# Optimization experiments

Hardware: AMD Instinct MI355X
Metric: run time of the kernel (lower is better)

## Reference

```python
import jax, jax.numpy as jnp
import numpy as np

# Config (matches init_kwargs)
B, S = 2, 2048            # 2 packed sequences of 2048 tokens (prefill)
HQ, HK, D = 32, 8, 128    # GQA: 32 query heads, 8 kv heads
G = HQ // HK              # group size 4
WINDOW = 1024             # sliding window
THETA = 10000.0


def setup_inputs() -> dict:
    key = jax.random.key(0)
    kq, kk, kv = jax.random.split(key, 3)
    n_tokens = B * S
    query = jax.random.normal(kq, (n_tokens, HQ * D), dtype=jnp.float32)
    key_t = jax.random.normal(kk, (n_tokens, HK * D), dtype=jnp.float32)
    value = jax.random.normal(kv, (n_tokens, HK * D), dtype=jnp.float32)
    # per-sequence positions restart at 0 for each packed sequence
    positions = jnp.tile(jnp.arange(S, dtype=jnp.int32), B)
    return {"query": query, "key": key_t, "value": value, "positions": positions}


def _rope(x, positions):
    # x: [B, S, H, D]; rotate-half (NeoX) RoPE
    half = D // 2
    inv_freq = 1.0 / (THETA ** (jnp.arange(0, half, dtype=jnp.float32) / half))
    ang = positions.astype(jnp.float32)[:, None] * inv_freq[None, :]   # [B*S, D/2]
    cos = jnp.cos(ang).reshape(B, S, 1, half)
    sin = jnp.sin(ang).reshape(B, S, 1, half)
    x1, x2 = x[..., :half], x[..., half:]
    return jnp.concatenate([x1 * cos - x2 * sin, x2 * cos + x1 * sin], axis=-1)


def reference(query, key, value, positions):
    q = query.reshape(B, S, HQ, D)
    k = key.reshape(B, S, HK, D)
    v = value.reshape(B, S, HK, D)
    q = _rope(q, positions)
    k = _rope(k, positions)
    # GQA: split q heads into [HK, G]
    qg = q.reshape(B, S, HK, G, D)
    scale = 1.0 / jnp.sqrt(jnp.float32(D))
    # scores: [B, HK, G, Sq, Skv]
    scores = jnp.einsum('bqhgd,bshd->bhgqs', qg, k) * scale
    i = jnp.arange(S)[:, None]
    j = jnp.arange(S)[None, :]
    # causal + sliding window: j <= i and i - j < WINDOW
    mask = (j <= i) & ((i - j) < WINDOW)
    scores = jnp.where(mask[None, None, None], scores, jnp.float32(-1e30))
    attn = jax.nn.softmax(scores, axis=-1)
    out = jnp.einsum('bhgqs,bshd->bqhgd', attn, v)   # [B, Sq, HK, G, D]
    return out.reshape(B * S, HQ * D)
```

## Files before the change

kernel.cpp:

```cpp
#include <hip/hip_runtime.h>
#include <stdint.h>

#define NB 2
#define NS 2048
#define NHK 8
#define ND 128
#define NWIN 1024

using bf16x8 = __bf16 __attribute__((ext_vector_type(8)));
using f32x4  = float  __attribute__((ext_vector_type(4)));
using f32x2  = float  __attribute__((ext_vector_type(2)));
using f32x8  = float  __attribute__((ext_vector_type(8)));
using u16x8  = unsigned short __attribute__((ext_vector_type(8)));
using u32x4  = unsigned int   __attribute__((ext_vector_type(4)));

#define L2_10K (13.287712379549449f / 64.0f)
#define MASKV (-3.0e38f)

static __device__ __forceinline__ float ex2(float x) {
  return __builtin_amdgcn_exp2f(x);
}

static __device__ __forceinline__ unsigned short f2bf(float x) {
  unsigned int u = __builtin_bit_cast(unsigned int, x);
  u += 0x7FFFu + ((u >> 16) & 1u);
  return (unsigned short)(u >> 16);
}

static __device__ __forceinline__ unsigned int cvtpk(float lo, float hi) {
  unsigned int r;
  asm("v_cvt_pk_bf16_f32 %0, %1, %2" : "=v"(r) : "v"(lo), "v"(hi));
  return r;
}

static __device__ __forceinline__ void gll16(const void* g, void* l) {
  __builtin_amdgcn_global_load_lds(
      (const __attribute__((address_space(1))) void*)g,
      (__attribute__((address_space(3))) void*)l, 16, 0, 0);
}

#define MFMA16(a, b, c) __builtin_amdgcn_mfma_f32_16x16x32_bf16((a), (b), (c), 0, 0, 0)

__global__ __launch_bounds__(64) void build_tab(float* __restrict__ tab) {
  const int p = blockIdx.x, f = threadIdx.x;
  float s, c;
  __sincosf((float)p * ex2(-(float)f * L2_10K), &s, &c);
  tab[(size_t)p * 128 + f] = c;
  tab[(size_t)p * 128 + 64 + f] = s;
}

__global__ __launch_bounds__(256) void prepass(
    const float* __restrict__ kin, const float* __restrict__ vin,
    const int* __restrict__ pos, const float* __restrict__ tab,
    unsigned short* __restrict__ kimg, unsigned short* __restrict__ vimg) {
  const int bid = blockIdx.x;
  const int ti = bid & 63, gidx = bid >> 6;
  const int hk = gidx & 7, b = gidx >> 3;
  const int t = threadIdx.x;

  unsigned short* kout = kimg + (size_t)bid * 4096;
#pragma unroll
  for (int uu = 0; uu < 2; ++uu) {
    const int u = t * 2 + uu;
    const int j = u >> 4;
    const int d0 = ((u & 15) << 3) ^ ((j & 7) << 3);
    const int tok = (b << 11) + (ti << 5) + j;
    const float* kp = kin + (size_t)tok * (NHK * ND) + hk * ND;
    f32x8 a = *(const f32x8*)(kp + d0);
    f32x8 p = *(const f32x8*)(kp + (d0 ^ 64));
    const float* tr = tab + (size_t)(pos[tok] & 2047) * 128 + (d0 & 63);
    f32x8 c8 = *(const f32x8*)tr;
    f32x8 s8 = *(const f32x8*)(tr + 64);
    u16x8 o;
#pragma unroll
    for (int i = 0; i < 8; ++i) {
      float val = (d0 < 64) ? (a[i] * c8[i] - p[i] * s8[i])
                            : (a[i] * c8[i] + p[i] * s8[i]);
      o[i] = f2bf(val);
    }
    *(u16x8*)(kout + (size_t)u * 8) = o;
  }

  unsigned short* vout = vimg + (size_t)bid * 4096;
  {
    const int d0 = (t >> 2) << 1;
    const int kp4 = t & 3;
    const int tok0 = (b << 11) + (ti << 5) + (kp4 << 3);
    const float* vp = vin + (size_t)tok0 * (NHK * ND) + hk * ND + d0;
    u16x8 lo, hi;
#pragma unroll
    for (int i = 0; i < 8; ++i) {
      f32x2 r = *(const f32x2*)(vp + (size_t)i * (NHK * ND));
      lo[i] = f2bf(r[0]);
      hi[i] = f2bf(r[1]);
    }
    const int sub = kp4 ^ ((d0 >> 1) & 3);
    *(u16x8*)(vout + d0 * 32 + sub * 8) = lo;
    *(u16x8*)(vout + (d0 + 1) * 32 + sub * 8) = hi;
  }
}

template <bool PRE>
__global__ __launch_bounds__(256, 3) void attn_fwd(
    const float* __restrict__ qin, const float* __restrict__ kin,
    const float* __restrict__ vin, const int* __restrict__ pos,
    const char* __restrict__ kimg, const char* __restrict__ vimg,
    const float* __restrict__ tab, float* __restrict__ out) {
  __shared__ __align__(16) char Kb[3][8192];
  __shared__ __align__(16) char Vb[3][8192];

  const int B = blockIdx.x;
  const int group = (B & 7) + ((B >> 9) << 3);
  const int qt = 63 - ((B >> 3) & 63);
  const int hk = group & 7, b = group >> 3;

  const int tid = threadIdx.x;
  const int w = tid >> 6, lane = tid & 63, h = lane >> 4, ln = lane & 15;
  const int g = w;
  const int q0b = qt << 5;
  int lo = q0b - (NWIN - 1);
  if (lo < 0) lo = 0;
  lo &= ~31;
  const int ti0 = lo >> 5;
  const int nt = (q0b >> 5) - ti0 + 1;

  const size_t gbase = (size_t)group * 64 * 8192;
  const char* kg = PRE ? kimg + gbase + (size_t)(w * 128 + lane) * 16 : nullptr;
  const char* vg = PRE ? vimg + gbase + (size_t)(w * 128 + lane) * 16 : nullptr;

  auto stage = [&](int sl, int ti) {
    if constexpr (PRE) {
      const char* ksrc = kg + (size_t)ti * 8192;
      const char* vsrc = vg + (size_t)ti * 8192;
      char* kd = &Kb[sl][w * 2048];
      char* vd = &Vb[sl][w * 2048];
      gll16(ksrc, kd);
      gll16(ksrc + 1024, kd + 1024);
      gll16(vsrc, vd);
      gll16(vsrc + 1024, vd + 1024);
    } else {
      const int j = tid >> 3;
      const int du = (tid & 7) << 4;
      const int tok = (b << 11) + (ti << 5) + j;
      const float* kp = kin + (size_t)tok * (NHK * ND) + hk * ND;
      const float pj = (float)pos[tok];
#pragma unroll
      for (int gq = 0; gq < 2; ++gq) {
        const int dd = du + gq * 8;
        f32x8 a = *(const f32x8*)(kp + dd);
        f32x8 p = *(const f32x8*)(kp + (dd ^ 64));
        u16x8 o;
#pragma unroll
        for (int i = 0; i < 8; ++i) {
          float s, c;
          __sincosf(pj * ex2(-(float)((dd & 63) + i) * L2_10K), &s, &c);
          float val = (dd < 64) ? (a[i] * c - p[i] * s) : (a[i] * c + p[i] * s);
          o[i] = f2bf(val);
        }
        *(u16x8*)(&Kb[sl][((j << 8) + (dd << 1)) ^ ((j & 7) << 4)]) = o;
      }
      const int d0 = (tid >> 2) << 1;
      const int kp4 = tid & 3;
      const float* vp = vin + (size_t)((b << 11) + (ti << 5) + (kp4 << 3)) * (NHK * ND) + hk * ND + d0;
      u16x8 lov, hiv;
#pragma unroll
      for (int i = 0; i < 8; ++i) {
        f32x2 r = *(const f32x2*)(vp + (size_t)i * (NHK * ND));
        lov[i] = f2bf(r[0]);
        hiv[i] = f2bf(r[1]);
      }
      const int sub = kp4 ^ ((d0 >> 1) & 3);
      unsigned short* vb16 = (unsigned short*)Vb[sl];
      *(u16x8*)(vb16 + d0 * 32 + sub * 8) = lov;
      *(u16x8*)(vb16 + (d0 + 1) * 32 + sub * 8) = hiv;
    }
  };

  stage(0, ti0);
  if (nt > 1) stage(1, ti0 + 1);

  const float QSC = 0.08838834764831845f * 1.4426950408889634f;
  bf16x8 qfr[2][4];
#pragma unroll
  for (int hf = 0; hf < 2; ++hf) {
    const int qrow = q0b + hf * 16 + ln;
    const size_t tokq = (size_t)(b << 11) + qrow;
    const float* qp = qin + tokq * 4096 + (hk * 4 + g) * 128;
    const int posq = pos[tokq] & 2047;
#pragma unroll
    for (int pp = 0; pp < 2; ++pp) {
      const int rr = (pp << 5) + (h << 3);
      f32x8 lo8 = *(const f32x8*)(qp + rr);
      f32x8 hi8 = *(const f32x8*)(qp + rr + 64);
      f32x8 cc, ss;
      if constexpr (PRE) {
        const float* tp = tab + (size_t)posq * 128 + rr;
        cc = *(const f32x8*)tp;
        ss = *(const f32x8*)(tp + 64);
      } else {
        const float pf = (float)posq;
#pragma unroll
        for (int i = 0; i < 8; ++i) {
          float s, c;
          __sincosf(pf * ex2(-(float)(rr + i) * L2_10K), &s, &c);
          cc[i] = c;
          ss[i] = s;
        }
      }
      u16x8 ulo, uhi;
#pragma unroll
      for (int i = 0; i < 8; ++i) {
        ulo[i] = f2bf((lo8[i] * cc[i] - hi8[i] * ss[i]) * QSC);
        uhi[i] = f2bf((hi8[i] * cc[i] + lo8[i] * ss[i]) * QSC);
      }
      qfr[hf][pp] = __builtin_bit_cast(bf16x8, ulo);
      qfr[hf][2 + pp] = __builtin_bit_cast(bf16x8, uhi);
    }
  }

  asm volatile("s_waitcnt vmcnt(0)" ::: "memory");

  f32x4 Oc[2][8] = {};
  float msh[2] = {-1e30f, -1e30f};
  float lsum[2] = {};
  const int sw = (ln & 7) << 4;
  const int vsub = (h ^ ((ln >> 1) & 3)) << 4;
  int s0 = 0, s1 = 1, s2 = 2;

  for (int t = 0; t < nt; ++t) {
    if constexpr (PRE) {
      if (t + 1 < nt) asm volatile("s_waitcnt vmcnt(4)" ::: "memory");
      else            asm volatile("s_waitcnt vmcnt(0)" ::: "memory");
    } else {
      asm volatile("s_waitcnt vmcnt(0) lgkmcnt(0)" ::: "memory");
    }
    __builtin_amdgcn_s_barrier();
    __builtin_amdgcn_sched_barrier(0);
    if (t + 2 < nt) stage(s2, ti0 + t + 2);

    const int j0 = (ti0 + t) << 5;
    const char* KB = Kb[s0];

    f32x4 sT[2][2] = {};
    __builtin_amdgcn_s_setprio(1);
#pragma unroll
    for (int c = 0; c < 4; ++c) {
      const bf16x8 k0 = *(const bf16x8*)(
          KB + (((ln << 8) + (c << 6) + (h << 4)) ^ sw));
      const bf16x8 k1 = *(const bf16x8*)(
          KB + ((((16 + ln) << 8) + (c << 6) + (h << 4)) ^ sw));
      sT[0][0] = MFMA16(k0, qfr[0][c], sT[0][0]);
      sT[0][1] = MFMA16(k1, qfr[0][c], sT[0][1]);
      sT[1][0] = MFMA16(k0, qfr[1][c], sT[1][0]);
      sT[1][1] = MFMA16(k1, qfr[1][c], sT[1][1]);
    }
    __builtin_amdgcn_s_setprio(0);

    if ((j0 >= q0b) || (j0 < q0b - 992)) {
#pragma unroll
      for (int qh = 0; qh < 2; ++qh) {
        const int irow = q0b + qh * 16 + ln;
#pragma unroll
        for (int ki = 0; ki < 2; ++ki)
#pragma unroll
          for (int r = 0; r < 4; ++r) {
            const int j = j0 + ki * 16 + (h << 2) + r;
            if (!(j <= irow && irow - j < NWIN)) sT[qh][ki][r] = MASKV;
          }
      }
    }

    float pm[2];
#pragma unroll
    for (int qh = 0; qh < 2; ++qh) {
      const f32x4 a0 = sT[qh][0], a1 = sT[qh][1];
      pm[qh] = fmaxf(fmaxf(fmaxf(a0[0], a0[1]), fmaxf(a0[2], a0[3])),
                     fmaxf(fmaxf(a1[0], a1[1]), fmaxf(a1[2], a1[3])));
    }
    const float ov = fmaxf(pm[0] - msh[0], pm[1] - msh[1]);
    if (__any(ov > 8.0f)) {
#pragma unroll
      for (int qh = 0; qh < 2; ++qh) {
        float M = pm[qh];
        M = fmaxf(M, __shfl_xor(M, 16));
        M = fmaxf(M, __shfl_xor(M, 32));
        const float mn = fmaxf(msh[qh], M);
        const float co = ex2(msh[qh] - mn);
        msh[qh] = mn;
        lsum[qh] *= co;
        float coO[4];
#pragma unroll
        for (int r = 0; r < 4; ++r) coO[r] = __shfl(co, (h << 2) + r);
#pragma unroll
        for (int db = 0; db < 8; ++db)
#pragma unroll
          for (int r = 0; r < 4; ++r) Oc[qh][db][r] *= coO[r];
      }
    }

    bf16x8 pa[2];
#pragma unroll
    for (int qh = 0; qh < 2; ++qh) {
#pragma unroll
      for (int ki = 0; ki < 2; ++ki)
#pragma unroll
        for (int r = 0; r < 4; ++r)
          sT[qh][ki][r] = ex2(sT[qh][ki][r] - msh[qh]);
      lsum[qh] += ((sT[qh][0][0] + sT[qh][0][1]) + (sT[qh][0][2] + sT[qh][0][3])) +
                  ((sT[qh][1][0] + sT[qh][1][1]) + (sT[qh][1][2] + sT[qh][1][3]));
      unsigned int A = cvtpk(sT[qh][0][0], sT[qh][0][1]);
      unsigned int Bk = cvtpk(sT[qh][0][2], sT[qh][0][3]);
      unsigned int C = cvtpk(sT[qh][1][0], sT[qh][1][1]);
      unsigned int D = cvtpk(sT[qh][1][2], sT[qh][1][3]);
      asm volatile("v_permlane32_swap_b32 %0, %1" : "+v"(A), "+v"(C));
      asm volatile("v_permlane16_swap_b32 %0, %1" : "+v"(A), "+v"(C));
      asm volatile("v_permlane32_swap_b32 %0, %1" : "+v"(Bk), "+v"(D));
      asm volatile("v_permlane16_swap_b32 %0, %1" : "+v"(Bk), "+v"(D));
      u32x4 pk4 = {A, Bk, C, D};
      pa[qh] = __builtin_bit_cast(bf16x8, pk4);
    }

    const char* VB = Vb[s0];
    __builtin_amdgcn_s_setprio(1);
#pragma unroll
    for (int db = 0; db < 8; ++db) {
      const bf16x8 vv = *(const bf16x8*)(VB + (db << 10) + (ln << 6) + vsub);
      Oc[0][db] = MFMA16(pa[0], vv, Oc[0][db]);
      Oc[1][db] = MFMA16(pa[1], vv, Oc[1][db]);
    }
    __builtin_amdgcn_s_setprio(0);

    const int tmp = s0;
    s0 = s1; s1 = s2; s2 = tmp;
  }

#pragma unroll
  for (int qh = 0; qh < 2; ++qh) {
    float ls = lsum[qh];
    ls += __shfl_xor(ls, 16);
    ls += __shfl_xor(ls, 32);
#pragma unroll
    for (int r = 0; r < 4; ++r) {
      const float rl = 1.0f / __shfl(ls, (h << 2) + r);
      const int irow = q0b + qh * 16 + (h << 2) + r;
      float* op = out + ((size_t)(b << 11) + irow) * 4096 + (hk * 4 + g) * 128 + ln;
#pragma unroll
      for (int db = 0; db < 8; ++db) op[db * 16] = Oc[qh][db][r] * rl;
    }
  }
}

extern "C" void kernel_launch(void* const* d_in, const int* in_sizes, int n_in,
                              void* d_out, int out_size, void* d_ws, size_t ws_size,
                              hipStream_t stream) {
  const float* q = (const float*)d_in[0];
  const float* k = (const float*)d_in[1];
  const float* v = (const float*)d_in[2];
  const int* pos = (const int*)d_in[3];
  float* out = (float*)d_out;

  const size_t TAB = (size_t)2048 * 128 * 4;
  const size_t KIMG = (size_t)16 * 64 * 8192;
  const size_t need = TAB + 2 * KIMG;

  if (ws_size >= need) {
    float* tab = (float*)d_ws;
    char* kimg = (char*)d_ws + TAB;
    char* vimg = kimg + KIMG;
    build_tab<<<2048, 64, 0, stream>>>(tab);
    prepass<<<1024, 256, 0, stream>>>(k, v, pos, tab,
                                      (unsigned short*)kimg, (unsigned short*)vimg);
    attn_fwd<true><<<1024, 256, 0, stream>>>(q, k, v, pos, kimg, vimg, tab, out);
  } else {
    attn_fwd<false><<<1024, 256, 0, stream>>>(q, k, v, pos, nullptr, nullptr, nullptr, out);
  }
}
```

Measured before the change: 95.92 us.

## Switch attention inner loop to 32x32x16 MFMA with double-buffered LDS

Replaces the 16x16x32 bf16 MFMA tiling with 32x32x16 MFMA for both QK^T and PV. Each lane now owns one query row, so the softmax max and sum reductions need only one cross-half shuffle, and output is written with vectorized float4 stores. The LDS pipeline goes from triple to double buffering with a __syncthreads per tile. That frees LDS for an occupancy hint of 4 blocks per CU but loses one stage of prefetch depth. Query tiles are also interleaved long and short to balance work across blocks.

```diff
diff --git a/kernel.cpp b/kernel.cpp
--- a/kernel.cpp
+++ b/kernel.cpp
@@ -11,6 +11,7 @@
 using f32x4  = float  __attribute__((ext_vector_type(4)));
 using f32x2  = float  __attribute__((ext_vector_type(2)));
 using f32x8  = float  __attribute__((ext_vector_type(8)));
+using f32x16 = float  __attribute__((ext_vector_type(16)));
 using u16x8  = unsigned short __attribute__((ext_vector_type(8)));
 using u32x4  = unsigned int   __attribute__((ext_vector_type(4)));
 
@@ -39,7 +40,7 @@
       (__attribute__((address_space(3))) void*)l, 16, 0, 0);
 }
 
-#define MFMA16(a, b, c) __builtin_amdgcn_mfma_f32_16x16x32_bf16((a), (b), (c), 0, 0, 0)
+#define MFMA32(a, b, c) __builtin_amdgcn_mfma_f32_32x32x16_bf16((a), (b), (c), 0, 0, 0)
 
 __global__ __launch_bounds__(64) void build_tab(float* __restrict__ tab) {
   const int p = blockIdx.x, f = threadIdx.x;
@@ -101,21 +102,23 @@
 }
 
 template <bool PRE>
-__global__ __launch_bounds__(256, 3) void attn_fwd(
+__global__ __launch_bounds__(256, 4) void attn_fwd(
     const float* __restrict__ qin, const float* __restrict__ kin,
     const float* __restrict__ vin, const int* __restrict__ pos,
     const char* __restrict__ kimg, const char* __restrict__ vimg,
     const float* __restrict__ tab, float* __restrict__ out) {
-  __shared__ __align__(16) char Kb[3][8192];
-  __shared__ __align__(16) char Vb[3][8192];
+  __shared__ __align__(16) char Kb[2][8192];
+  __shared__ __align__(16) char Vb[2][8192];
 
   const int B = blockIdx.x;
   const int group = (B & 7) + ((B >> 9) << 3);
-  const int qt = 63 - ((B >> 3) & 63);
+  const int qi = (B >> 3) & 63;
+  const int qt = (qi & 1) ? (qi >> 1) : (63 - (qi >> 1));
   const int hk = group & 7, b = group >> 3;
 
   const int tid = threadIdx.x;
-  const int w = tid >> 6, lane = tid & 63, h = lane >> 4, ln = lane & 15;
+  const int w = tid >> 6, lane = tid & 63;
+  const int r32 = lane & 31, hi = lane >> 5;
   const int g = w;
   const int q0b = qt << 5;
   int lo = q0b - (NWIN - 1);
@@ -124,20 +127,17 @@
   const int ti0 = lo >> 5;
   const int nt = (q0b >> 5) - ti0 + 1;
 
-  const size_t gbase = (size_t)group * 64 * 8192;
-  const char* kg = PRE ? kimg + gbase + (size_t)(w * 128 + lane) * 16 : nullptr;
-  const char* vg = PRE ? vimg + gbase + (size_t)(w * 128 + lane) * 16 : nullptr;
+  const int gvoff = group * 64 * 8192 + (w * 128 + lane) * 16;
 
   auto stage = [&](int sl, int ti) {
     if constexpr (PRE) {
-      const char* ksrc = kg + (size_t)ti * 8192;
-      const char* vsrc = vg + (size_t)ti * 8192;
+      const int off = gvoff + ti * 8192;
       char* kd = &Kb[sl][w * 2048];
       char* vd = &Vb[sl][w * 2048];
-      gll16(ksrc, kd);
-      gll16(ksrc + 1024, kd + 1024);
-      gll16(vsrc, vd);
-      gll16(vsrc + 1024, vd + 1024);
+      gll16(kimg + off, kd);
+      gll16(kimg + off + 1024, kd + 1024);
+      gll16(vimg + off, vd);
+      gll16(vimg + off + 1024, vd + 1024);
     } else {
       const int j = tid >> 3;
       const int du = (tid & 7) << 4;
@@ -177,24 +177,22 @@
   };
 
   stage(0, ti0);
-  if (nt > 1) stage(1, ti0 + 1);
 
   const float QSC = 0.08838834764831845f * 1.4426950408889634f;
-  bf16x8 qfr[2][4];
-#pragma unroll
-  for (int hf = 0; hf < 2; ++hf) {
-    const int qrow = q0b + hf * 16 + ln;
+  bf16x8 qfr[8];
+  {
+    const int qrow = q0b + r32;
     const size_t tokq = (size_t)(b << 11) + qrow;
     const float* qp = qin + tokq * 4096 + (hk * 4 + g) * 128;
     const int posq = pos[tokq] & 2047;
 #pragma unroll
-    for (int pp = 0; pp < 2; ++pp) {
-      const int rr = (pp << 5) + (h << 3);
-      f32x8 lo8 = *(const f32x8*)(qp + rr);
-      f32x8 hi8 = *(const f32x8*)(qp + rr + 64);
+    for (int m = 0; m < 4; ++m) {
+      const int dlo = (m << 4) + (hi << 3);
+      f32x8 lo8 = *(const f32x8*)(qp + dlo);
+      f32x8 hi8 = *(const f32x8*)(qp + dlo + 64);
       f32x8 cc, ss;
       if constexpr (PRE) {
-        const float* tp = tab + (size_t)posq * 128 + rr;
+        const float* tp = tab + (size_t)posq * 128 + dlo;
         cc = *(const f32x8*)tp;
         ss = *(const f32x8*)(tp + 64);
       } else {
@@ -202,7 +200,7 @@
 #pragma unroll
         for (int i = 0; i < 8; ++i) {
           float s, c;
-          __sincosf(pf * ex2(-(float)(rr + i) * L2_10K), &s, &c);
+          __sincosf(pf * ex2(-(float)(dlo + i) * L2_10K), &s, &c);
           cc[i] = c;
           ss[i] = s;
         }
@@ -213,141 +211,99 @@
         ulo[i] = f2bf((lo8[i] * cc[i] - hi8[i] * ss[i]) * QSC);
         uhi[i] = f2bf((hi8[i] * cc[i] + lo8[i] * ss[i]) * QSC);
       }
-      qfr[hf][pp] = __builtin_bit_cast(bf16x8, ulo);
-      qfr[hf][2 + pp] = __builtin_bit_cast(bf16x8, uhi);
-    }
-  }
-
-  asm volatile("s_waitcnt vmcnt(0)" ::: "memory");
-
-  f32x4 Oc[2][8] = {};
-  float msh[2] = {-1e30f, -1e30f};
-  float lsum[2] = {};
-  const int sw = (ln & 7) << 4;
-  const int vsub = (h ^ ((ln >> 1) & 3)) << 4;
-  int s0 = 0, s1 = 1, s2 = 2;
+      qfr[m] = __builtin_bit_cast(bf16x8, ulo);
+      qfr[m + 4] = __builtin_bit_cast(bf16x8, uhi);
+    }
+  }
+
+  f32x16 Oc[4] = {};
+  float msh = -1e30f;
+  float lsum = 0.0f;
+
+  const int kx = (r32 << 8) | ((hi ^ (r32 & 1)) << 4) | (((r32 & 7) >> 1) << 5);
+  const int vsz = (r32 >> 1) & 3;
+  const int vbase0 = r32 * 64;
 
   for (int t = 0; t < nt; ++t) {
-    if constexpr (PRE) {
-      if (t + 1 < nt) asm volatile("s_waitcnt vmcnt(4)" ::: "memory");
-      else            asm volatile("s_waitcnt vmcnt(0)" ::: "memory");
-    } else {
-      asm volatile("s_waitcnt vmcnt(0) lgkmcnt(0)" ::: "memory");
-    }
-    __builtin_amdgcn_s_barrier();
-    __builtin_amdgcn_sched_barrier(0);
-    if (t + 2 < nt) stage(s2, ti0 + t + 2);
+    __syncthreads();
+    if (t + 1 < nt) stage((t + 1) & 1, ti0 + t + 1);
 
     const int j0 = (ti0 + t) << 5;
-    const char* KB = Kb[s0];
-
-    f32x4 sT[2][2] = {};
+    const char* KB = Kb[t & 1];
+    const char* VB = Vb[t & 1];
+
+    f32x16 sT = {};
     __builtin_amdgcn_s_setprio(1);
 #pragma unroll
-    for (int c = 0; c < 4; ++c) {
-      const bf16x8 k0 = *(const bf16x8*)(
-          KB + (((ln << 8) + (c << 6) + (h << 4)) ^ sw));
-      const bf16x8 k1 = *(const bf16x8*)(
-          KB + ((((16 + ln) << 8) + (c << 6) + (h << 4)) ^ sw));
-      sT[0][0] = MFMA16(k0, qfr[0][c], sT[0][0]);
-      sT[0][1] = MFMA16(k1, qfr[0][c], sT[0][1]);
-      sT[1][0] = MFMA16(k0, qfr[1][c], sT[1][0]);
-      sT[1][1] = MFMA16(k1, qfr[1][c], sT[1][1]);
+    for (int m = 0; m < 8; ++m) {
+      const bf16x8 kf = *(const bf16x8*)(KB + (kx ^ (m << 5)));
+      sT = MFMA32(kf, qfr[m], sT);
     }
     __builtin_amdgcn_s_setprio(0);
 
     if ((j0 >= q0b) || (j0 < q0b - 992)) {
-#pragma unroll
-      for (int qh = 0; qh < 2; ++qh) {
-        const int irow = q0b + qh * 16 + ln;
-#pragma unroll
-        for (int ki = 0; ki < 2; ++ki)
-#pragma unroll
-          for (int r = 0; r < 4; ++r) {
-            const int j = j0 + ki * 16 + (h << 2) + r;
-            if (!(j <= irow && irow - j < NWIN)) sT[qh][ki][r] = MASKV;
-          }
-      }
-    }
-
-    float pm[2];
-#pragma unroll
-    for (int qh = 0; qh < 2; ++qh) {
-      const f32x4 a0 = sT[qh][0], a1 = sT[qh][1];
-      pm[qh] = fmaxf(fmaxf(fmaxf(a0[0], a0[1]), fmaxf(a0[2], a0[3])),
-                     fmaxf(fmaxf(a1[0], a1[1]), fmaxf(a1[2], a1[3])));
-    }
-    const float ov = fmaxf(pm[0] - msh[0], pm[1] - msh[1]);
-    if (__any(ov > 8.0f)) {
-#pragma unroll
-      for (int qh = 0; qh < 2; ++qh) {
-        float M = pm[qh];
-        M = fmaxf(M, __shfl_xor(M, 16));
-        M = fmaxf(M, __shfl_xor(M, 32));
-        const float mn = fmaxf(msh[qh], M);
-        const float co = ex2(msh[qh] - mn);
-        msh[qh] = mn;
-        lsum[qh] *= co;
-        float coO[4];
-#pragma unroll
-        for (int r = 0; r < 4; ++r) coO[r] = __shfl(co, (h << 2) + r);
-#pragma unroll
-        for (int db = 0; db < 8; ++db)
-#pragma unroll
-          for (int r = 0; r < 4; ++r) Oc[qh][db][r] *= coO[r];
-      }
-    }
-
-    bf16x8 pa[2];
-#pragma unroll
-    for (int qh = 0; qh < 2; ++qh) {
-#pragma unroll
-      for (int ki = 0; ki < 2; ++ki)
-#pragma unroll
-        for (int r = 0; r < 4; ++r)
-          sT[qh][ki][r] = ex2(sT[qh][ki][r] - msh[qh]);
-      lsum[qh] += ((sT[qh][0][0] + sT[qh][0][1]) + (sT[qh][0][2] + sT[qh][0][3])) +
-                  ((sT[qh][1][0] + sT[qh][1][1]) + (sT[qh][1][2] + sT[qh][1][3]));
-      unsigned int A = cvtpk(sT[qh][0][0], sT[qh][0][1]);
-      unsigned int Bk = cvtpk(sT[qh][0][2], sT[qh][0][3]);
-      unsigned int C = cvtpk(sT[qh][1][0], sT[qh][1][1]);
-      unsigned int D = cvtpk(sT[qh][1][2], sT[qh][1][3]);
-      asm volatile("v_permlane32_swap_b32 %0, %1" : "+v"(A), "+v"(C));
-      asm volatile("v_permlane16_swap_b32 %0, %1" : "+v"(A), "+v"(C));
-      asm volatile("v_permlane32_swap_b32 %0, %1" : "+v"(Bk), "+v"(D));
-      asm volatile("v_permlane16_swap_b32 %0, %1" : "+v"(Bk), "+v"(D));
-      u32x4 pk4 = {A, Bk, C, D};
-      pa[qh] = __builtin_bit_cast(bf16x8, pk4);
-    }
-
-    const char* VB = Vb[s0];
+      const int irow = q0b + r32;
+#pragma unroll
+      for (int r = 0; r < 16; ++r) {
+        const int j = j0 + (r & 3) + 8 * (r >> 2) + 4 * hi;
+        if (!(j <= irow && irow - j < NWIN)) sT[r] = MASKV;
+      }
+    }
+
+    float pm = sT[0];
+#pragma unroll
+    for (int r = 1; r < 16; ++r) pm = fmaxf(pm, sT[r]);
+    if (__any(pm - msh > 8.0f)) {
+      float M = fmaxf(pm, __shfl_xor(pm, 32));
+      const float mn = fmaxf(msh, M);
+      const float co = ex2(msh - mn);
+      msh = mn;
+      lsum *= co;
+#pragma unroll
+      for (int dt = 0; dt < 4; ++dt)
+#pragma unroll
+        for (int r = 0; r < 16; ++r) Oc[dt][r] *= co;
+    }
+#pragma unroll
+    for (int r = 0; r < 16; ++r) sT[r] = ex2(sT[r] - msh);
+    lsum += (((sT[0] + sT[1]) + (sT[2] + sT[3])) + ((sT[4] + sT[5]) + (sT[6] + sT[7]))) +
+            (((sT[8] + sT[9]) + (sT[10] + sT[11])) + ((sT[12] + sT[13]) + (sT[14] + sT[15])));
+
+    unsigned int A00 = cvtpk(sT[0], sT[1]),   A01 = cvtpk(sT[2], sT[3]);
+    unsigned int A10 = cvtpk(sT[4], sT[5]),   A11 = cvtpk(sT[6], sT[7]);
+    unsigned int A20 = cvtpk(sT[8], sT[9]),   A21 = cvtpk(sT[10], sT[11]);
+    unsigned int A30 = cvtpk(sT[12], sT[13]), A31 = cvtpk(sT[14], sT[15]);
+
     __builtin_amdgcn_s_setprio(1);
 #pragma unroll
-    for (int db = 0; db < 8; ++db) {
-      const bf16x8 vv = *(const bf16x8*)(VB + (db << 10) + (ln << 6) + vsub);
-      Oc[0][db] = MFMA16(pa[0], vv, Oc[0][db]);
-      Oc[1][db] = MFMA16(pa[1], vv, Oc[1][db]);
+    for (int ks = 0; ks < 2; ++ks) {
+      unsigned int w0 = ks ? A20 : A00, w1 = ks ? A21 : A01;
+      unsigned int w2 = ks ? A30 : A10, w3 = ks ? A31 : A11;
+      asm volatile("v_permlane32_swap_b32 %0, %1" : "+v"(w0), "+v"(w2));
+      asm volatile("v_permlane32_swap_b32 %0, %1" : "+v"(w1), "+v"(w3));
+      u32x4 pk4 = {w0, w1, w2, w3};
+      const bf16x8 pb = __builtin_bit_cast(bf16x8, pk4);
+      const int vslot = (((ks << 1) | hi) ^ vsz) << 4;
+#pragma unroll
+      for (int dt = 0; dt < 4; ++dt) {
+        const bf16x8 vf = *(const bf16x8*)(VB + (dt << 11) + vbase0 + vslot);
+        Oc[dt] = MFMA32(vf, pb, Oc[dt]);
+      }
     }
     __builtin_amdgcn_s_setprio(0);
-
-    const int tmp = s0;
-    s0 = s1; s1 = s2; s2 = tmp;
-  }
-
-#pragma unroll
-  for (int qh = 0; qh < 2; ++qh) {
-    float ls = lsum[qh];
-    ls += __shfl_xor(ls, 16);
-    ls += __shfl_xor(ls, 32);
-#pragma unroll
-    for (int r = 0; r < 4; ++r) {
-      const float rl = 1.0f / __shfl(ls, (h << 2) + r);
-      const int irow = q0b + qh * 16 + (h << 2) + r;
-      float* op = out + ((size_t)(b << 11) + irow) * 4096 + (hk * 4 + g) * 128 + ln;
-#pragma unroll
-      for (int db = 0; db < 8; ++db) op[db * 16] = Oc[qh][db][r] * rl;
-    }
-  }
+  }
+
+  float ls = lsum + __shfl_xor(lsum, 32);
+  const float rl = 1.0f / ls;
+  float* op = out + ((size_t)(b << 11) + q0b + r32) * 4096 + (hk * 4 + g) * 128 + (hi << 2);
+#pragma unroll
+  for (int dt = 0; dt < 4; ++dt)
+#pragma unroll
+    for (int s = 0; s < 4; ++s) {
+      f32x4 o = {Oc[dt][4 * s + 0] * rl, Oc[dt][4 * s + 1] * rl,
+                 Oc[dt][4 * s + 2] * rl, Oc[dt][4 * s + 3] * rl};
+      *(f32x4*)(op + (dt << 5) + (s << 3)) = o;
+    }
 }
 
 extern "C" void kernel_launch(void* const* d_in, const int* in_sizes, int n_in,
```

Result: slower. 137.7 us (+43.5%).

## Load V fragments directly from global into registers, double-buffer K only

Applied to the files above, without the earlier changes.

V tiles are no longer staged through LDS. Each lane now loads its bf16 V fragments straight from the preformatted global image into registers, split into two halves around the softmax. K staging drops from a triple-buffer ring to a double buffer with a full vmcnt(0) wait and syncthreads each iteration. The aim is to cut LDS footprint and LDS traffic, but the V global-load latency is now exposed inside the loop and the prefetch depth is reduced.

```diff
diff --git a/kernel.cpp b/kernel.cpp
--- a/kernel.cpp
+++ b/kernel.cpp
@@ -106,8 +106,7 @@
     const float* __restrict__ vin, const int* __restrict__ pos,
     const char* __restrict__ kimg, const char* __restrict__ vimg,
     const float* __restrict__ tab, float* __restrict__ out) {
-  __shared__ __align__(16) char Kb[3][8192];
-  __shared__ __align__(16) char Vb[3][8192];
+  __shared__ __align__(16) char Kb[2][8192];
 
   const int B = blockIdx.x;
   const int group = (B & 7) + ((B >> 9) << 3);
@@ -126,18 +125,14 @@
 
   const size_t gbase = (size_t)group * 64 * 8192;
   const char* kg = PRE ? kimg + gbase + (size_t)(w * 128 + lane) * 16 : nullptr;
-  const char* vg = PRE ? vimg + gbase + (size_t)(w * 128 + lane) * 16 : nullptr;
+  const char* vgb = PRE ? vimg + gbase : nullptr;
 
   auto stage = [&](int sl, int ti) {
     if constexpr (PRE) {
       const char* ksrc = kg + (size_t)ti * 8192;
-      const char* vsrc = vg + (size_t)ti * 8192;
       char* kd = &Kb[sl][w * 2048];
-      char* vd = &Vb[sl][w * 2048];
       gll16(ksrc, kd);
       gll16(ksrc + 1024, kd + 1024);
-      gll16(vsrc, vd);
-      gll16(vsrc + 1024, vd + 1024);
     } else {
       const int j = tid >> 3;
       const int du = (tid & 7) << 4;
@@ -159,25 +154,10 @@
         }
         *(u16x8*)(&Kb[sl][((j << 8) + (dd << 1)) ^ ((j & 7) << 4)]) = o;
       }
-      const int d0 = (tid >> 2) << 1;
-      const int kp4 = tid & 3;
-      const float* vp = vin + (size_t)((b << 11) + (ti << 5) + (kp4 << 3)) * (NHK * ND) + hk * ND + d0;
-      u16x8 lov, hiv;
-#pragma unroll
-      for (int i = 0; i < 8; ++i) {
-        f32x2 r = *(const f32x2*)(vp + (size_t)i * (NHK * ND));
-        lov[i] = f2bf(r[0]);
-        hiv[i] = f2bf(r[1]);
-      }
-      const int sub = kp4 ^ ((d0 >> 1) & 3);
-      unsigned short* vb16 = (unsigned short*)Vb[sl];
-      *(u16x8*)(vb16 + d0 * 32 + sub * 8) = lov;
-      *(u16x8*)(vb16 + (d0 + 1) * 32 + sub * 8) = hiv;
     }
   };
 
   stage(0, ti0);
-  if (nt > 1) stage(1, ti0 + 1);
 
   const float QSC = 0.08838834764831845f * 1.4426950408889634f;
   bf16x8 qfr[2][4];
@@ -218,28 +198,37 @@
     }
   }
 
-  asm volatile("s_waitcnt vmcnt(0)" ::: "memory");
-
   f32x4 Oc[2][8] = {};
   float msh[2] = {-1e30f, -1e30f};
   float lsum[2] = {};
   const int sw = (ln & 7) << 4;
-  const int vsub = (h ^ ((ln >> 1) & 3)) << 4;
-  int s0 = 0, s1 = 1, s2 = 2;
+  const int voff = (ln << 6) + ((h ^ ((ln >> 1) & 3)) << 4);
 
   for (int t = 0; t < nt; ++t) {
+    asm volatile("s_waitcnt vmcnt(0)" ::: "memory");
+    __syncthreads();
+    if (t + 1 < nt) stage((t + 1) & 1, ti0 + t + 1);
+
+    const int j0 = (ti0 + t) << 5;
+    const char* KB = Kb[t & 1];
+    const char* vt = PRE ? vgb + (size_t)(ti0 + t) * 8192 : nullptr;
+
+    bf16x8 vf[8];
     if constexpr (PRE) {
-      if (t + 1 < nt) asm volatile("s_waitcnt vmcnt(4)" ::: "memory");
-      else            asm volatile("s_waitcnt vmcnt(0)" ::: "memory");
+#pragma unroll
+      for (int db = 0; db < 4; ++db)
+        vf[db] = *(const bf16x8*)(vt + (db << 10) + voff);
     } else {
-      asm volatile("s_waitcnt vmcnt(0) lgkmcnt(0)" ::: "memory");
-    }
-    __builtin_amdgcn_s_barrier();
-    __builtin_amdgcn_sched_barrier(0);
-    if (t + 2 < nt) stage(s2, ti0 + t + 2);
-
-    const int j0 = (ti0 + t) << 5;
-    const char* KB = Kb[s0];
+#pragma unroll
+      for (int db = 0; db < 4; ++db) {
+        u16x8 o;
+#pragma unroll
+        for (int i = 0; i < 8; ++i)
+          o[i] = f2bf(vin[(size_t)((b << 11) + j0 + (h << 3) + i) * (NHK * ND) +
+                          hk * ND + (db << 4) + ln]);
+        vf[db] = __builtin_bit_cast(bf16x8, o);
+      }
+    }
 
     f32x4 sT[2][2] = {};
     __builtin_amdgcn_s_setprio(1);
@@ -320,18 +309,29 @@
       pa[qh] = __builtin_bit_cast(bf16x8, pk4);
     }
 
-    const char* VB = Vb[s0];
+    if constexpr (PRE) {
+#pragma unroll
+      for (int db = 4; db < 8; ++db)
+        vf[db] = *(const bf16x8*)(vt + (db << 10) + voff);
+    } else {
+#pragma unroll
+      for (int db = 4; db < 8; ++db) {
+        u16x8 o;
+#pragma unroll
+        for (int i = 0; i < 8; ++i)
+          o[i] = f2bf(vin[(size_t)((b << 11) + j0 + (h << 3) + i) * (NHK * ND) +
+                          hk * ND + (db << 4) + ln]);
+        vf[db] = __builtin_bit_cast(bf16x8, o);
+      }
+    }
+
     __builtin_amdgcn_s_setprio(1);
 #pragma unroll
     for (int db = 0; db < 8; ++db) {
-      const bf16x8 vv = *(const bf16x8*)(VB + (db << 10) + (ln << 6) + vsub);
-      Oc[0][db] = MFMA16(pa[0], vv, Oc[0][db]);
-      Oc[1][db] = MFMA16(pa[1], vv, Oc[1][db]);
+      Oc[0][db] = MFMA16(pa[0], vf[db], Oc[0][db]);
+      Oc[1][db] = MFMA16(pa[1], vf[db], Oc[1][db]);
     }
     __builtin_amdgcn_s_setprio(0);
-
-    const int tmp = s0;
-    s0 = s1; s1 = s2; s2 = tmp;
   }
 
 #pragma unroll
```

After: 103.3 us. 7.7% more time.

## Pair short and long causal query tiles per block and double-buffer K/V

Applied to the files above, without the earlier changes.

The grid shrinks from 1024 to 768 blocks. Each of the first 16 units per group handles two query tiles, a short early one (qt=u) and a long late one (qt=31-u), so the ramp-up region of the causal mask is balanced. The remaining units handle one full-window tile each. The K/V shared staging drops from triple to double buffering, which frees LDS but waits on all outstanding loads plus a full __syncthreads every iteration, reducing load/compute overlap. The intent is to even out per-block work across the causal/windowed workload.

```diff
diff --git a/kernel.cpp b/kernel.cpp
--- a/kernel.cpp
+++ b/kernel.cpp
@@ -106,23 +106,22 @@
     const float* __restrict__ vin, const int* __restrict__ pos,
     const char* __restrict__ kimg, const char* __restrict__ vimg,
     const float* __restrict__ tab, float* __restrict__ out) {
-  __shared__ __align__(16) char Kb[3][8192];
-  __shared__ __align__(16) char Vb[3][8192];
+  __shared__ __align__(16) char Kb[2][8192];
+  __shared__ __align__(16) char Vb[2][8192];
 
   const int B = blockIdx.x;
-  const int group = (B & 7) + ((B >> 9) << 3);
-  const int qt = 63 - ((B >> 3) & 63);
+  const int xcd = B & 7;
+  const int i96 = B >> 3;
+  const int group = xcd + ((i96 >= 48) ? 8 : 0);
+  const int unit = (i96 >= 48) ? i96 - 48 : i96;
   const int hk = group & 7, b = group >> 3;
+  const int isPair = unit < 16;
+  const int qtA = isPair ? unit : unit + 16;
+  const int qtB = 31 - unit;
 
   const int tid = threadIdx.x;
   const int w = tid >> 6, lane = tid & 63, h = lane >> 4, ln = lane & 15;
   const int g = w;
-  const int q0b = qt << 5;
-  int lo = q0b - (NWIN - 1);
-  if (lo < 0) lo = 0;
-  lo &= ~31;
-  const int ti0 = lo >> 5;
-  const int nt = (q0b >> 5) - ti0 + 1;
 
   const size_t gbase = (size_t)group * 64 * 8192;
   const char* kg = PRE ? kimg + gbase + (size_t)(w * 128 + lane) * 16 : nullptr;
@@ -176,176 +175,178 @@
     }
   };
 
-  stage(0, ti0);
-  if (nt > 1) stage(1, ti0 + 1);
-
   const float QSC = 0.08838834764831845f * 1.4426950408889634f;
-  bf16x8 qfr[2][4];
-#pragma unroll
-  for (int hf = 0; hf < 2; ++hf) {
-    const int qrow = q0b + hf * 16 + ln;
-    const size_t tokq = (size_t)(b << 11) + qrow;
-    const float* qp = qin + tokq * 4096 + (hk * 4 + g) * 128;
-    const int posq = pos[tokq] & 2047;
-#pragma unroll
-    for (int pp = 0; pp < 2; ++pp) {
-      const int rr = (pp << 5) + (h << 3);
-      f32x8 lo8 = *(const f32x8*)(qp + rr);
-      f32x8 hi8 = *(const f32x8*)(qp + rr + 64);
-      f32x8 cc, ss;
-      if constexpr (PRE) {
-        const float* tp = tab + (size_t)posq * 128 + rr;
-        cc = *(const f32x8*)tp;
-        ss = *(const f32x8*)(tp + 64);
-      } else {
-        const float pf = (float)posq;
-#pragma unroll
-        for (int i = 0; i < 8; ++i) {
-          float s, c;
-          __sincosf(pf * ex2(-(float)(rr + i) * L2_10K), &s, &c);
-          cc[i] = c;
-          ss[i] = s;
-        }
-      }
-      u16x8 ulo, uhi;
-#pragma unroll
-      for (int i = 0; i < 8; ++i) {
-        ulo[i] = f2bf((lo8[i] * cc[i] - hi8[i] * ss[i]) * QSC);
-        uhi[i] = f2bf((hi8[i] * cc[i] + lo8[i] * ss[i]) * QSC);
-      }
-      qfr[hf][pp] = __builtin_bit_cast(bf16x8, ulo);
-      qfr[hf][2 + pp] = __builtin_bit_cast(bf16x8, uhi);
-    }
-  }
-
-  asm volatile("s_waitcnt vmcnt(0)" ::: "memory");
-
-  f32x4 Oc[2][8] = {};
-  float msh[2] = {-1e30f, -1e30f};
-  float lsum[2] = {};
   const int sw = (ln & 7) << 4;
   const int vsub = (h ^ ((ln >> 1) & 3)) << 4;
-  int s0 = 0, s1 = 1, s2 = 2;
-
-  for (int t = 0; t < nt; ++t) {
-    if constexpr (PRE) {
-      if (t + 1 < nt) asm volatile("s_waitcnt vmcnt(4)" ::: "memory");
-      else            asm volatile("s_waitcnt vmcnt(0)" ::: "memory");
-    } else {
-      asm volatile("s_waitcnt vmcnt(0) lgkmcnt(0)" ::: "memory");
-    }
-    __builtin_amdgcn_s_barrier();
-    __builtin_amdgcn_sched_barrier(0);
-    if (t + 2 < nt) stage(s2, ti0 + t + 2);
-
-    const int j0 = (ti0 + t) << 5;
-    const char* KB = Kb[s0];
-
-    f32x4 sT[2][2] = {};
-    __builtin_amdgcn_s_setprio(1);
-#pragma unroll
-    for (int c = 0; c < 4; ++c) {
-      const bf16x8 k0 = *(const bf16x8*)(
-          KB + (((ln << 8) + (c << 6) + (h << 4)) ^ sw));
-      const bf16x8 k1 = *(const bf16x8*)(
-          KB + ((((16 + ln) << 8) + (c << 6) + (h << 4)) ^ sw));
-      sT[0][0] = MFMA16(k0, qfr[0][c], sT[0][0]);
-      sT[0][1] = MFMA16(k1, qfr[0][c], sT[0][1]);
-      sT[1][0] = MFMA16(k0, qfr[1][c], sT[1][0]);
-      sT[1][1] = MFMA16(k1, qfr[1][c], sT[1][1]);
-    }
-    __builtin_amdgcn_s_setprio(0);
-
-    if ((j0 >= q0b) || (j0 < q0b - 992)) {
+
+#pragma unroll 1
+  for (int seg = 0; seg < 2; ++seg) {
+    if (seg == 1 && !isPair) break;
+    const int qt = seg ? qtB : qtA;
+    const int q0b = qt << 5;
+    int lo = q0b - (NWIN - 1);
+    if (lo < 0) lo = 0;
+    lo &= ~31;
+    const int ti0 = lo >> 5;
+    const int nt = (q0b >> 5) - ti0 + 1;
+
+    __syncthreads();
+    stage(0, ti0);
+
+    bf16x8 qfr[2][4];
+#pragma unroll
+    for (int hf = 0; hf < 2; ++hf) {
+      const int qrow = q0b + hf * 16 + ln;
+      const size_t tokq = (size_t)(b << 11) + qrow;
+      const float* qp = qin + tokq * 4096 + (hk * 4 + g) * 128;
+      const int posq = pos[tokq] & 2047;
+#pragma unroll
+      for (int pp = 0; pp < 2; ++pp) {
+        const int rr = (pp << 5) + (h << 3);
+        f32x8 lo8 = *(const f32x8*)(qp + rr);
+        f32x8 hi8 = *(const f32x8*)(qp + rr + 64);
+        f32x8 cc, ss;
+        if constexpr (PRE) {
+          const float* tp = tab + (size_t)posq * 128 + rr;
+          cc = *(const f32x8*)tp;
+          ss = *(const f32x8*)(tp + 64);
+        } else {
+          const float pf = (float)posq;
+#pragma unroll
+          for (int i = 0; i < 8; ++i) {
+            float s, c;
+            __sincosf(pf * ex2(-(float)(rr + i) * L2_10K), &s, &c);
+            cc[i] = c;
+            ss[i] = s;
+          }
+        }
+        u16x8 ulo, uhi;
+#pragma unroll
+        for (int i = 0; i < 8; ++i) {
+          ulo[i] = f2bf((lo8[i] * cc[i] - hi8[i] * ss[i]) * QSC);
+          uhi[i] = f2bf((hi8[i] * cc[i] + lo8[i] * ss[i]) * QSC);
+        }
+        qfr[hf][pp] = __builtin_bit_cast(bf16x8, ulo);
+        qfr[hf][2 + pp] = __builtin_bit_cast(bf16x8, uhi);
+      }
+    }
+
+    f32x4 Oc[2][8] = {};
+    float msh[2] = {-1e30f, -1e30f};
+    float lsum[2] = {};
+
+#pragma unroll 1
+    for (int t = 0; t < nt; ++t) {
+      asm volatile("s_waitcnt vmcnt(0)" ::: "memory");
+      __syncthreads();
+      if (t + 1 < nt) stage((t + 1) & 1, ti0 + t + 1);
+
+      const int j0 = (ti0 + t) << 5;
+      const char* KB = Kb[t & 1];
+
+      f32x4 sT[2][2] = {};
+      __builtin_amdgcn_s_setprio(1);
+#pragma unroll
+      for (int c = 0; c < 4; ++c) {
+        const bf16x8 k0 = *(const bf16x8*)(
+            KB + (((ln << 8) + (c << 6) + (h << 4)) ^ sw));
+        const bf16x8 k1 = *(const bf16x8*)(
+            KB + ((((16 + ln) << 8) + (c << 6) + (h << 4)) ^ sw));
+        sT[0][0] = MFMA16(k0, qfr[0][c], sT[0][0]);
+        sT[0][1] = MFMA16(k1, qfr[0][c], sT[0][1]);
+        sT[1][0] = MFMA16(k0, qfr[1][c], sT[1][0]);
+        sT[1][1] = MFMA16(k1, qfr[1][c], sT[1][1]);
+      }
+      __builtin_amdgcn_s_setprio(0);
+
+      if ((j0 >= q0b) || (j0 < q0b - 992)) {
+#pragma unroll
+        for (int qh = 0; qh < 2; ++qh) {
+          const int irow = q0b + qh * 16 + ln;
+#pragma unroll
+          for (int ki = 0; ki < 2; ++ki)
+#pragma unroll
+            for (int r = 0; r < 4; ++r) {
+              const int j = j0 + ki * 16 + (h << 2) + r;
+              if (!(j <= irow && irow - j < NWIN)) sT[qh][ki][r] = MASKV;
+            }
+        }
+      }
+
+      float pm[2];
 #pragma unroll
       for (int qh = 0; qh < 2; ++qh) {
-        const int irow = q0b + qh * 16 + ln;
+        const f32x4 a0 = sT[qh][0], a1 = sT[qh][1];
+        pm[qh] = fmaxf(fmaxf(fmaxf(a0[0], a0[1]), fmaxf(a0[2], a0[3])),
+                       fmaxf(fmaxf(a1[0], a1[1]), fmaxf(a1[2], a1[3])));
+      }
+      const float ov = fmaxf(pm[0] - msh[0], pm[1] - msh[1]);
+      if (__any(ov > 8.0f)) {
+#pragma unroll
+        for (int qh = 0; qh < 2; ++qh) {
+          float M = pm[qh];
+          M = fmaxf(M, __shfl_xor(M, 16));
+          M = fmaxf(M, __shfl_xor(M, 32));
+          const float mn = fmaxf(msh[qh], M);
+          const float co = ex2(msh[qh] - mn);
+          msh[qh] = mn;
+          lsum[qh] *= co;
+          float coO[4];
+#pragma unroll
+          for (int r = 0; r < 4; ++r) coO[r] = __shfl(co, (h << 2) + r);
+#pragma unroll
+          for (int db = 0; db < 8; ++db)
+#pragma unroll
+            for (int r = 0; r < 4; ++r) Oc[qh][db][r] *= coO[r];
+        }
+      }
+
+      bf16x8 pa[2];
+#pragma unroll
+      for (int qh = 0; qh < 2; ++qh) {
 #pragma unroll
         for (int ki = 0; ki < 2; ++ki)
 #pragma unroll
-          for (int r = 0; r < 4; ++r) {
-            const int j = j0 + ki * 16 + (h << 2) + r;
-            if (!(j <= irow && irow - j < NWIN)) sT[qh][ki][r] = MASKV;
-          }
-      }
-    }
-
-    float pm[2];
+          for (int r = 0; r < 4; ++r)
+            sT[qh][ki][r] = ex2(sT[qh][ki][r] - msh[qh]);
+        lsum[qh] += ((sT[qh][0][0] + sT[qh][0][1]) + (sT[qh][0][2] + sT[qh][0][3])) +
+                    ((sT[qh][1][0] + sT[qh][1][1]) + (sT[qh][1][2] + sT[qh][1][3]));
+        unsigned int A = cvtpk(sT[qh][0][0], sT[qh][0][1]);
+        unsigned int Bk = cvtpk(sT[qh][0][2], sT[qh][0][3]);
+        unsigned int C = cvtpk(sT[qh][1][0], sT[qh][1][1]);
+        unsigned int D = cvtpk(sT[qh][1][2], sT[qh][1][3]);
+        asm volatile("v_permlane32_swap_b32 %0, %1" : "+v"(A), "+v"(C));
+        asm volatile("v_permlane16_swap_b32 %0, %1" : "+v"(A), "+v"(C));
+        asm volatile("v_permlane32_swap_b32 %0, %1" : "+v"(Bk), "+v"(D));
+        asm volatile("v_permlane16_swap_b32 %0, %1" : "+v"(Bk), "+v"(D));
+        u32x4 pk4 = {A, Bk, C, D};
+        pa[qh] = __builtin_bit_cast(bf16x8, pk4);
+      }
+
+      const char* VB = Vb[t & 1];
+      __builtin_amdgcn_s_setprio(1);
+#pragma unroll
+      for (int db = 0; db < 8; ++db) {
+        const bf16x8 vv = *(const bf16x8*)(VB + (db << 10) + (ln << 6) + vsub);
+        Oc[0][db] = MFMA16(pa[0], vv, Oc[0][db]);
+        Oc[1][db] = MFMA16(pa[1], vv, Oc[1][db]);
+      }
+      __builtin_amdgcn_s_setprio(0);
+    }
+
 #pragma unroll
     for (int qh = 0; qh < 2; ++qh) {
-      const f32x4 a0 = sT[qh][0], a1 = sT[qh][1];
-      pm[qh] = fmaxf(fmaxf(fmaxf(a0[0], a0[1]), fmaxf(a0[2], a0[3])),
-                     fmaxf(fmaxf(a1[0], a1[1]), fmaxf(a1[2], a1[3])));
-    }
-    const float ov = fmaxf(pm[0] - msh[0], pm[1] - msh[1]);
-    if (__any(ov > 8.0f)) {
-#pragma unroll
-      for (int qh = 0; qh < 2; ++qh) {
-        float M = pm[qh];
-        M = fmaxf(M, __shfl_xor(M, 16));
-        M = fmaxf(M, __shfl_xor(M, 32));
-        const float mn = fmaxf(msh[qh], M);
-        const float co = ex2(msh[qh] - mn);
-        msh[qh] = mn;
-        lsum[qh] *= co;
-        float coO[4];
-#pragma unroll
-        for (int r = 0; r < 4; ++r) coO[r] = __shfl(co, (h << 2) + r);
-#pragma unroll
-        for (int db = 0; db < 8; ++db)
-#pragma unroll
-          for (int r = 0; r < 4; ++r) Oc[qh][db][r] *= coO[r];
-      }
-    }
-
-    bf16x8 pa[2];
-#pragma unroll
-    for (int qh = 0; qh < 2; ++qh) {
-#pragma unroll
-      for (int ki = 0; ki < 2; ++ki)
-#pragma unroll
-        for (int r = 0; r < 4; ++r)
-          sT[qh][ki][r] = ex2(sT[qh][ki][r] - msh[qh]);
-      lsum[qh] += ((sT[qh][0][0] + sT[qh][0][1]) + (sT[qh][0][2] + sT[qh][0][3])) +
-                  ((sT[qh][1][0] + sT[qh][1][1]) + (sT[qh][1][2] + sT[qh][1][3]));
-      unsigned int A = cvtpk(sT[qh][0][0], sT[qh][0][1]);
-      unsigned int Bk = cvtpk(sT[qh][0][2], sT[qh][0][3]);
-      unsigned int C = cvtpk(sT[qh][1][0], sT[qh][1][1]);
-      unsigned int D = cvtpk(sT[qh][1][2], sT[qh][1][3]);
-      asm volatile("v_permlane32_swap_b32 %0, %1" : "+v"(A), "+v"(C));
-      asm volatile("v_permlane16_swap_b32 %0, %1" : "+v"(A), "+v"(C));
-      asm volatile("v_permlane32_swap_b32 %0, %1" : "+v"(Bk), "+v"(D));
-      asm volatile("v_permlane16_swap_b32 %0, %1" : "+v"(Bk), "+v"(D));
-      u32x4 pk4 = {A, Bk, C, D};
-      pa[qh] = __builtin_bit_cast(bf16x8, pk4);
-    }
-
-    const char* VB = Vb[s0];
-    __builtin_amdgcn_s_setprio(1);
-#pragma unroll
-    for (int db = 0; db < 8; ++db) {
-      const bf16x8 vv = *(const bf16x8*)(VB + (db << 10) + (ln << 6) + vsub);
-      Oc[0][db] = MFMA16(pa[0], vv, Oc[0][db]);
-      Oc[1][db] = MFMA16(pa[1], vv, Oc[1][db]);
-    }
-    __builtin_amdgcn_s_setprio(0);
-
-    const int tmp = s0;
-    s0 = s1; s1 = s2; s2 = tmp;
-  }
-
-#pragma unroll
-  for (int qh = 0; qh < 2; ++qh) {
-    float ls = lsum[qh];
-    ls += __shfl_xor(ls, 16);
-    ls += __shfl_xor(ls, 32);
-#pragma unroll
-    for (int r = 0; r < 4; ++r) {
-      const float rl = 1.0f / __shfl(ls, (h << 2) + r);
-      const int irow = q0b + qh * 16 + (h << 2) + r;
-      float* op = out + ((size_t)(b << 11) + irow) * 4096 + (hk * 4 + g) * 128 + ln;
-#pragma unroll
-      for (int db = 0; db < 8; ++db) op[db * 16] = Oc[qh][db][r] * rl;
+      float ls = lsum[qh];
+      ls += __shfl_xor(ls, 16);
+      ls += __shfl_xor(ls, 32);
+#pragma unroll
+      for (int r = 0; r < 4; ++r) {
+        const float rl = 1.0f / __shfl(ls, (h << 2) + r);
+        const int irow = q0b + qh * 16 + (h << 2) + r;
+        float* op = out + ((size_t)(b << 11) + irow) * 4096 + (hk * 4 + g) * 128 + ln;
+#pragma unroll
+        for (int db = 0; db < 8; ++db) op[db * 16] = Oc[qh][db][r] * rl;
+      }
     }
   }
 }
@@ -370,8 +371,8 @@
     build_tab<<<2048, 64, 0, stream>>>(tab);
     prepass<<<1024, 256, 0, stream>>>(k, v, pos, tab,
                                       (unsigned short*)kimg, (unsigned short*)vimg);
-    attn_fwd<true><<<1024, 256, 0, stream>>>(q, k, v, pos, kimg, vimg, tab, out);
+    attn_fwd<true><<<768, 256, 0, stream>>>(q, k, v, pos, kimg, vimg, tab, out);
   } else {
-    attn_fwd<false><<<1024, 256, 0, stream>>>(q, k, v, pos, nullptr, nullptr, nullptr, out);
+    attn_fwd<false><<<768, 256, 0, stream>>>(q, k, v, pos, nullptr, nullptr, nullptr, out);
   }
 }
```

After: 95.13 us. Within noise of the previous version (-0.8%).
